# Performance work log

Measured on AMD Instinct MI355X. Metric: run time of the kernel, lower is better.

## Reference

```python
import jax, jax.numpy as jnp
import numpy as np

N = 50000   # nodes
E = 800000  # edges
D = 512     # channels (hidden_dim*2 == input_dim)
B = 64      # graphs in batch
L = 4       # GCN layers
OUT = 2
EPS = 1e-5


def setup_inputs() -> dict:
    key = jax.random.key(0)
    ks = jax.random.split(key, 12)
    x = jax.random.normal(ks[0], (N, D), jnp.float32)
    edge_index = jax.random.randint(ks[1], (2, E), 0, N, dtype=jnp.int64)
    batch = jnp.sort(jax.random.randint(ks[2], (N,), 0, B, dtype=jnp.int64))
    same_date = jax.random.randint(ks[3], (E,), 0, 2, dtype=jnp.int64)
    # parameters: 4 stacked GCNConv layers (same shape), BN stats, final linear
    Wc = jax.random.normal(ks[4], (L, D, D), jnp.float32) / np.float32(np.sqrt(D))
    bc = jax.random.normal(ks[5], (L, D), jnp.float32) * 0.01
    gamma = 1.0 + 0.1 * jax.random.normal(ks[6], (L, D), jnp.float32)
    beta = 0.1 * jax.random.normal(ks[7], (L, D), jnp.float32)
    rmean = 0.1 * jax.random.normal(ks[8], (L, D), jnp.float32)
    rvar = 0.5 + jax.random.uniform(ks[9], (L, D), jnp.float32)
    Wlin = jax.random.normal(ks[10], (2 * D, OUT), jnp.float32) / np.float32(np.sqrt(2 * D))
    blin = jnp.zeros((OUT,), jnp.float32)
    return {"x": x, "edge_index": edge_index, "batch": batch, "same_date": same_date,
            "Wc": Wc, "bc": bc, "gamma": gamma, "beta": beta, "rmean": rmean,
            "rvar": rvar, "Wlin": Wlin, "blin": blin}


def reference(x, edge_index, batch, same_date, Wc, bc, gamma, beta, rmean, rvar, Wlin, blin):
    # edge weights: 1.0 if same_date else 0.7
    w = jnp.where(same_date == 1, jnp.float32(1.0), jnp.float32(0.7))
    # GCN normalization with added self-loops (fill value 1.0)
    loops = jnp.arange(N, dtype=edge_index.dtype)
    row = jnp.concatenate([edge_index[0], loops])  # sources
    col = jnp.concatenate([edge_index[1], loops])  # targets
    ew = jnp.concatenate([w, jnp.ones((N,), jnp.float32)])
    deg = jax.ops.segment_sum(ew, col, num_segments=N)          # in-degree (weighted)
    dis = jax.lax.rsqrt(jnp.maximum(deg, EPS))                   # deg >= 1 from self-loops
    norm = dis[row] * ew * dis[col]                              # [E+N]

    h = x
    for i in range(L):
        hw = h @ Wc[i]                                           # [N, D]
        msg = hw[row] * norm[:, None]                            # gather + scale
        agg = jax.ops.segment_sum(msg, col, num_segments=N) + bc[i]
        # BatchNorm (inference: running stats) + ReLU; dropout is identity in eval
        h = gamma[i] * (agg - rmean[i]) * jax.lax.rsqrt(rvar[i] + EPS) + beta[i]
        h = jax.nn.relu(h)

    counts = jax.ops.segment_sum(jnp.ones((N,), jnp.float32), batch, num_segments=B)
    x_mean = jax.ops.segment_sum(h, batch, num_segments=B) / jnp.maximum(counts, 1.0)[:, None]
    x_max = jax.ops.segment_max(h, batch, num_segments=B)
    x_max = jnp.where(jnp.isfinite(x_max), x_max, 0.0)           # guard empty graphs
    z = jnp.concatenate([x_mean, x_max], axis=1) @ Wlin + blin   # [B, OUT]
    return jax.nn.log_softmax(z, axis=1)
```

## Files before the change

kernel.cpp:

```cpp
#include <hip/hip_runtime.h>
#include <hip/hip_bf16.h>

#define NN 50000
#define EE 800000
#define DD 512
#define BB 64
#define LL 4
#define OUTC 2
#define EPSV 1e-5f

#define MTG 64
#define BKG 64
#define HV8 (NN * DD / 8)

typedef _Float16 halfx8 __attribute__((ext_vector_type(8)));
typedef float floatx4 __attribute__((ext_vector_type(4)));
typedef float floatx2 __attribute__((ext_vector_type(2)));

#if defined(__has_builtin)
#if __has_builtin(__builtin_amdgcn_cvt_pk_f32_fp8) && __has_builtin(__builtin_amdgcn_cvt_pk_fp8_f32)
#define HW_FP8 1
#endif
#endif

#ifdef HW_FP8
__device__ __forceinline__ floatx2 f8x2_lo(unsigned int u) {
    return __builtin_amdgcn_cvt_pk_f32_fp8(u, 0);
}
__device__ __forceinline__ floatx2 f8x2_hi(unsigned int u) {
    return __builtin_amdgcn_cvt_pk_f32_fp8(u, 1);
}
__device__ __forceinline__ unsigned int f8_pack_lo(float a, float b, unsigned int old) {
    return (unsigned int)__builtin_amdgcn_cvt_pk_fp8_f32(a, b, (int)old, 0);
}
__device__ __forceinline__ unsigned int f8_pack_hi(float a, float b, unsigned int old) {
    return (unsigned int)__builtin_amdgcn_cvt_pk_fp8_f32(a, b, (int)old, 1);
}
__device__ __forceinline__ unsigned char f8_enc1(float v) {
    return (unsigned char)(__builtin_amdgcn_cvt_pk_fp8_f32(v, v, 0, 0) & 0xff);
}
#else
__device__ __forceinline__ float f8_dec1(unsigned int b) {
    unsigned int s = b & 0x80u, e = (b >> 3) & 15u, m = b & 7u;
    float v = e ? __uint_as_float(((e + 120u) << 23) | (m << 20))
                : (float)m * 0.001953125f;
    return s ? -v : v;
}
__device__ __forceinline__ floatx2 f8x2_lo(unsigned int u) {
    floatx2 r; r[0] = f8_dec1(u & 0xffu); r[1] = f8_dec1((u >> 8) & 0xffu); return r;
}
__device__ __forceinline__ floatx2 f8x2_hi(unsigned int u) {
    floatx2 r; r[0] = f8_dec1((u >> 16) & 0xffu); r[1] = f8_dec1((u >> 24) & 0xffu); return r;
}
__device__ __forceinline__ unsigned char f8_enc1(float x) {
    unsigned int s = (__float_as_uint(x) >> 24) & 0x80u;
    float a = fabsf(x);
    if (a < 0.015625f) {
        int m = (int)(a * 512.0f + 0.5f);
        return (unsigned char)(s | (unsigned int)m);
    }
    unsigned int ab = __float_as_uint(a);
    int e = (int)(ab >> 23) - 127;
    unsigned int m23 = ab & 0x7fffffu;
    unsigned int r = m23 + 0x7ffffu + ((m23 >> 20) & 1u);
    if (r >= 0x800000u) { e++; r -= 0x800000u; }
    unsigned int m = r >> 20;
    if (e > 8 || (e == 8 && m >= 7u)) return (unsigned char)(s | 0x7eu);
    return (unsigned char)(s | ((unsigned int)(e + 7) << 3) | m);
}
__device__ __forceinline__ unsigned int f8_pack_lo(float a, float b, unsigned int old) {
    return (old & 0xffff0000u) | (unsigned int)f8_enc1(a) | ((unsigned int)f8_enc1(b) << 8);
}
__device__ __forceinline__ unsigned int f8_pack_hi(float a, float b, unsigned int old) {
    return (old & 0x0000ffffu) | ((unsigned int)f8_enc1(a) << 16) | ((unsigned int)f8_enc1(b) << 24);
}
#endif

__device__ __forceinline__ floatx4 mfma16h(halfx8 a, halfx8 b, floatx4 c) {
    return __builtin_amdgcn_mfma_f32_16x16x32_f16(a, b, c, 0, 0, 0);
}

__device__ __forceinline__ void ldg2lds16(const _Float16* g, _Float16* l) {
    __builtin_amdgcn_global_load_lds(
        (const __attribute__((address_space(1))) unsigned int*)g,
        (__attribute__((address_space(3))) unsigned int*)l, 16, 0, 0);
}


__global__ void k_prep(const float* __restrict__ x, const float* __restrict__ Wc,
                       const int* __restrict__ ei, const int* __restrict__ sd,
                       const float* __restrict__ bc, const float* __restrict__ gamma,
                       const float* __restrict__ beta, const float* __restrict__ rmean,
                       const float* __restrict__ rvar,
                       unsigned char* __restrict__ X8, _Float16* __restrict__ WT,
                       unsigned long long* __restrict__ degcnt,
                       float* __restrict__ scb, float* __restrict__ shb) {
    int i = blockIdx.x * blockDim.x + threadIdx.x;
    if (i < HV8) {
        const float4* xp = (const float4*)x + (size_t)i * 2;
        float4 v0 = xp[0], v1 = xp[1];
        unsigned int u0 = 0, u1 = 0;
        u0 = f8_pack_lo(v0.x, v0.y, u0);
        u0 = f8_pack_hi(v0.z, v0.w, u0);
        u1 = f8_pack_lo(v1.x, v1.y, u1);
        u1 = f8_pack_hi(v1.z, v1.w, u1);
        uint2 q; q.x = u0; q.y = u1;
        ((uint2*)X8)[i] = q;
    }
    if (i < LL * DD * DD) {
        int l = i >> 18;
        int rem = i & ((DD * DD) - 1);
        int n = rem >> 9;
        int k = rem & (DD - 1);
        WT[(l << 18) + (n << 9) + (k ^ ((n & 7) << 3))] =
            (_Float16)Wc[(l << 18) + (k << 9) + n];
    }
    if (i < LL * DD) {
        float rs = rsqrtf(rvar[i] + EPSV);
        float scv = gamma[i] * rs;
        scb[i] = scv;
        shb[i] = scv * (bc[i] - rmean[i]) + beta[i];
    }
    if ((i & 3) == 0) {
        int e = i >> 2;
        if (e < EE) {
            int c = ei[EE + e];
            unsigned long long v =
                0x100000000ull + (unsigned long long)((sd[e] == 1) ? 10u : 7u);
            atomicAdd(&degcnt[c], v);
        }
    }
}

__global__ void k_scan1(const unsigned long long* __restrict__ degcnt,
                        int* __restrict__ rowptr, int* __restrict__ bsum,
                        float* __restrict__ dis, const int* __restrict__ batch,
                        int* __restrict__ gstart, int* __restrict__ gend) {
    __shared__ int sh[256];
    const int t = threadIdx.x;
    const int i = blockIdx.x * 256 + t;
    int cntv = 0;
    if (i < NN) {
        unsigned long long dc = degcnt[i];
        cntv = (int)(dc >> 32);
        float degv = 0.1f * (float)(unsigned int)(dc & 0xffffffffu);
        dis[i] = rsqrtf(fmaxf(degv + 1.0f, EPSV));
        int g = batch[i];
        int gp = (i == 0) ? -1 : batch[i - 1];
        if (g != gp) gstart[g] = i;
        int gn = (i == NN - 1) ? BB : batch[i + 1];
        if (g != gn) gend[g] = i + 1;
    }
    sh[t] = cntv;
    __syncthreads();
    for (int off = 1; off < 256; off <<= 1) {
        int y = (t >= off) ? sh[t - off] : 0;
        __syncthreads();
        if (t >= off) sh[t] += y;
        __syncthreads();
    }
    if (i < NN) rowptr[i] = sh[t] - cntv;
    if (t == 255) bsum[blockIdx.x] = sh[255];
}

__global__ void k_scan2(int* __restrict__ bsum, int* __restrict__ rowptr, int nb) {
    __shared__ int sh[256];
    const int t = threadIdx.x;
    int v = (t < nb) ? bsum[t] : 0;
    sh[t] = v;
    __syncthreads();
    for (int off = 1; off < 256; off <<= 1) {
        int y = (t >= off) ? sh[t - off] : 0;
        __syncthreads();
        if (t >= off) sh[t] += y;
        __syncthreads();
    }
    if (t < nb) bsum[t] = sh[t] - v;
    if (t == 255) rowptr[NN] = sh[255];
}

__global__ void k_scan3(int* __restrict__ rowptr, const int* __restrict__ bsum) {
    int i = blockIdx.x * blockDim.x + threadIdx.x;
    if (i < NN) rowptr[i] += bsum[i >> 8];
}

__global__ void k_fill(const int* __restrict__ ei, const int* __restrict__ sd,
                       const float* __restrict__ dis, const int* __restrict__ rowptr,
                       int* __restrict__ fill, int* __restrict__ srcs,
                       float* __restrict__ enorm) {
    int e = blockIdx.x * blockDim.x + threadIdx.x;
    if (e >= EE) return;
    int s = ei[e];
    int c = ei[EE + e];
    float w = (sd[e] == 1) ? 1.0f : 0.7f;
    int p = rowptr[c] + atomicAdd(&fill[c], 1);
    srcs[p] = s;
    enorm[p] = dis[s] * w * dis[c];
}

__launch_bounds__(256)
__global__ void k_agg(const unsigned char* __restrict__ h8, const int* __restrict__ rowptr,
                      const int* __restrict__ srcs, const float* __restrict__ enorm,
                      const float* __restrict__ dis, _Float16* __restrict__ S) {
    const int n = blockIdx.x * 4 + (threadIdx.x >> 6);
    const int lane = threadIdx.x & 63;
    if (n >= NN) return;
    const float dn = dis[n];
    const float sw = dn * dn;
    uint2 q = ((const uint2*)(h8 + (size_t)n * DD))[lane];
    floatx2 acc[4];
    acc[0] = f8x2_lo(q.x) * sw;
    acc[1] = f8x2_hi(q.x) * sw;
    acc[2] = f8x2_lo(q.y) * sw;
    acc[3] = f8x2_hi(q.y) * sw;
    const int s0 = rowptr[n], s1 = rowptr[n + 1];
    int i = s0;
    for (; i + 8 <= s1; i += 8) {
        int sv[8];
        float wv[8];
        uint2 qv[8];
#pragma unroll
        for (int u = 0; u < 8; u++) { sv[u] = srcs[i + u]; wv[u] = enorm[i + u]; }
#pragma unroll
        for (int u = 0; u < 8; u++)
            qv[u] = ((const uint2*)(h8 + (size_t)sv[u] * DD))[lane];
#pragma unroll
        for (int u = 0; u < 8; u++) {
            acc[0] += f8x2_lo(qv[u].x) * wv[u];
            acc[1] += f8x2_hi(qv[u].x) * wv[u];
            acc[2] += f8x2_lo(qv[u].y) * wv[u];
            acc[3] += f8x2_hi(qv[u].y) * wv[u];
        }
    }
    for (; i + 4 <= s1; i += 4) {
        int sv[4];
        float wv[4];
        uint2 qv[4];
#pragma unroll
        for (int u = 0; u < 4; u++) { sv[u] = srcs[i + u]; wv[u] = enorm[i + u]; }
#pragma unroll
        for (int u = 0; u < 4; u++)
            qv[u] = ((const uint2*)(h8 + (size_t)sv[u] * DD))[lane];
#pragma unroll
        for (int u = 0; u < 4; u++) {
            acc[0] += f8x2_lo(qv[u].x) * wv[u];
            acc[1] += f8x2_hi(qv[u].x) * wv[u];
            acc[2] += f8x2_lo(qv[u].y) * wv[u];
            acc[3] += f8x2_hi(qv[u].y) * wv[u];
        }
    }
    for (; i < s1; i++) {
        uint2 qb = ((const uint2*)(h8 + (size_t)srcs[i] * DD))[lane];
        const float wn = enorm[i];
        acc[0] += f8x2_lo(qb.x) * wn;
        acc[1] += f8x2_hi(qb.x) * wn;
        acc[2] += f8x2_lo(qb.y) * wn;
        acc[3] += f8x2_hi(qb.y) * wn;
    }
    halfx8 hv;
#pragma unroll
    for (int k = 0; k < 4; k++) {
        hv[2 * k] = (_Float16)acc[k][0];
        hv[2 * k + 1] = (_Float16)acc[k][1];
    }
    ((halfx8*)(S + (size_t)n * DD))[lane ^ (n & 7)] = hv;
}

template <int OUT8>
__launch_bounds__(512)
__global__ void k_gemm(const _Float16* __restrict__ A,
                       const _Float16* __restrict__ B,
                       const float* __restrict__ sc, const float* __restrict__ sh,
                       _Float16* __restrict__ C16, unsigned char* __restrict__ C8) {
    __shared__ _Float16 sA[MTG * BKG];
    __shared__ _Float16 sB[512 * BKG];

    const int t = threadIdx.x;
    const int wid = t >> 6;
    const int lane = t & 63;
    const int l15 = lane & 15;
    const int quad = lane >> 4;
    const int m0 = blockIdx.x * MTG;
    const int wc = wid * 64;
    const int key = l15 & 7;

    int arow = m0 + (t >> 3);
    if (arow > NN - 1) arow = NN - 1;
    const _Float16* gA = A + (size_t)arow * DD + (t & 7) * 8;
    _Float16* lA = sA + t * 8;
    const _Float16* gB = B + (size_t)(t >> 3) * DD + (t & 7) * 8;
    _Float16* lB = sB + t * 8;

    floatx4 acc[4][4];
#pragma unroll
    for (int i = 0; i < 4; i++)
#pragma unroll
        for (int j = 0; j < 4; j++) acc[i][j] = (floatx4){0.f, 0.f, 0.f, 0.f};

    for (int k0 = 0; k0 < DD; k0 += BKG) {
        __syncthreads();
        ldg2lds16(gA + k0, lA);
#pragma unroll
        for (int r = 0; r < 8; r++)
            ldg2lds16(gB + (size_t)r * 64 * DD + k0, lB + r * 4096);
        __syncthreads();

#pragma unroll
        for (int cc = 0; cc < 2; cc++) {
            halfx8 a[4], b[4];
            const int goff = ((cc * 4 + quad) ^ key) * 8;
#pragma unroll
            for (int i = 0; i < 4; i++)
                a[i] = *(const halfx8*)&sA[(i * 16 + l15) * BKG + goff];
#pragma unroll
            for (int j = 0; j < 4; j++)
                b[j] = *(const halfx8*)&sB[(wc + j * 16 + l15) * BKG + goff];
#pragma unroll
            for (int i = 0; i < 4; i++)
#pragma unroll
                for (int j = 0; j < 4; j++)
                    acc[i][j] = mfma16h(a[i], b[j], acc[i][j]);
        }
    }

#pragma unroll
    for (int j = 0; j < 4; j++) {
        const int gcol = wc + j * 16 + l15;
        const float scv = sc[gcol];
        const float shv = sh[gcol];
#pragma unroll
        for (int i = 0; i < 4; i++) {
            const int rbase = m0 + i * 16 + quad * 4;
#pragma unroll
            for (int r = 0; r < 4; r++) {
                const int grow = rbase + r;
                if (grow < NN) {
                    float v = fmaxf(fmaf(scv, acc[i][j][r], shv), 0.f);
                    if (OUT8)
                        C8[(size_t)grow * DD + gcol] = f8_enc1(v);
                    else
                        C16[(size_t)grow * DD + gcol] = (_Float16)v;
                }
            }
        }
    }
}

__launch_bounds__(512)
__global__ void k_pool(const _Float16* __restrict__ H,
                       const int* __restrict__ gstart, const int* __restrict__ gend,
                       float* __restrict__ psum, unsigned int* __restrict__ pmax) {
    const int g = blockIdx.x;
    const int sl = blockIdx.y;
    const int c = threadIdx.x;
    const int s0 = gstart[g], e0 = gend[g];
    if (e0 <= s0) return;
    const int len = e0 - s0;
    const int chunk = (len + 7) >> 3;
    const int lo = s0 + sl * chunk;
    const int hi = min(lo + chunk, e0);
    float sum = 0.f, mx = 0.f;
    for (int n = lo; n < hi; n++) {
        float v = (float)H[(size_t)n * DD + c];
        sum += v;
        mx = fmaxf(mx, v);
    }
    if (lo < hi) {
        atomicAdd(&psum[g * DD + c], sum);
        atomicMax(&pmax[g * DD + c], __float_as_uint(fmaxf(mx, 0.f)));
    }
}

__launch_bounds__(64)
__global__ void k_final(const float* __restrict__ psum, const unsigned int* __restrict__ pmax,
                        const int* __restrict__ gstart, const int* __restrict__ gend,
                        const float* __restrict__ Wlin, const float* __restrict__ blin,
                        float* __restrict__ out) {
    const int g = blockIdx.x;
    const int lane = threadIdx.x;
    int cntg = gend[g] - gstart[g];
    if (cntg < 1) cntg = 1;
    const float inv = 1.0f / (float)cntg;
    float z0 = 0.f, z1 = 0.f;
#pragma unroll
    for (int j = 0; j < 8; j++) {
        const int k = j * 64 + lane;
        float mean = psum[g * DD + k] * inv;
        float mx = __uint_as_float(pmax[g * DD + k]);
        z0 += mean * Wlin[k * OUTC + 0] + mx * Wlin[(DD + k) * OUTC + 0];
        z1 += mean * Wlin[k * OUTC + 1] + mx * Wlin[(DD + k) * OUTC + 1];
    }
#pragma unroll
    for (int off = 32; off > 0; off >>= 1) {
        z0 += __shfl_down(z0, off);
        z1 += __shfl_down(z1, off);
    }
    if (lane == 0) {
        z0 += blin[0];
        z1 += blin[1];
        float m = fmaxf(z0, z1);
        float ls = m + logf(expf(z0 - m) + expf(z1 - m));
        out[g * OUTC + 0] = z0 - ls;
        out[g * OUTC + 1] = z1 - ls;
    }
}

extern "C" void kernel_launch(void* const* d_in, const int* in_sizes, int n_in,
                              void* d_out, int out_size, void* d_ws, size_t ws_size,
                              hipStream_t stream) {
    const float* x = (const float*)d_in[0];
    const int* ei = (const int*)d_in[1];
    const int* batch = (const int*)d_in[2];
    const int* sd = (const int*)d_in[3];
    const float* Wc = (const float*)d_in[4];
    const float* bc = (const float*)d_in[5];
    const float* gamma = (const float*)d_in[6];
    const float* beta = (const float*)d_in[7];
    const float* rmean = (const float*)d_in[8];
    const float* rvar = (const float*)d_in[9];
    const float* Wlin = (const float*)d_in[10];
    const float* blin = (const float*)d_in[11];
    float* out = (float*)d_out;

    char* p = (char*)d_ws;
    auto alloc = [&](size_t bytes) {
        char* r = p;
        p += (bytes + 255) & ~(size_t)255;
        return r;
    };
    _Float16* S = (_Float16*)alloc((size_t)NN * DD * 2);
    unsigned char* X8a = (unsigned char*)alloc((size_t)NN * DD);
    unsigned char* X8b = (unsigned char*)alloc((size_t)NN * DD);
    _Float16* WT = (_Float16*)alloc((size_t)LL * DD * DD * 2);
    float* scb = (float*)alloc(LL * DD * 4);
    float* shb = (float*)alloc(LL * DD * 4);
    char* zbase = p;
    unsigned long long* degcnt = (unsigned long long*)alloc(NN * 8);
    float* dis = (float*)alloc(NN * 4);
    int* fill = (int*)alloc(NN * 4);
    int* rowptr = (int*)alloc((NN + 1) * 4);
    int* bsum = (int*)alloc(256 * 4);
    int* srcs = (int*)alloc(EE * 4);
    float* enorm = (float*)alloc(EE * 4);
    int* gstart = (int*)alloc(BB * 4);
    int* gend = (int*)alloc(BB * 4);
    float* psum = (float*)alloc(BB * DD * 4);
    unsigned int* pmax = (unsigned int*)alloc(BB * DD * 4);
    size_t zbytes = (size_t)(p - zbase);
    (void)ws_size; (void)in_sizes; (void)n_in; (void)out_size;

    const int nb256 = (NN + 255) / 256;
    const int eb256 = (EE + 255) / 256;

    hipMemsetAsync(zbase, 0, zbytes, stream);
    k_prep<<<(HV8 + 255) / 256, 256, 0, stream>>>(x, Wc, ei, sd, bc, gamma, beta,
                                                  rmean, rvar, X8a, WT, degcnt, scb, shb);
    k_scan1<<<nb256, 256, 0, stream>>>(degcnt, rowptr, bsum, dis, batch, gstart, gend);
    k_scan2<<<1, 256, 0, stream>>>(bsum, rowptr, nb256);
    k_scan3<<<nb256, 256, 0, stream>>>(rowptr, bsum);
    k_fill<<<eb256, 256, 0, stream>>>(ei, sd, dis, rowptr, fill, srcs, enorm);

    const int ggrid = (NN + MTG - 1) / MTG;
    unsigned char* bufs[2] = {X8a, X8b};
    int cur = 0;
    for (int l = 0; l < LL; l++) {
        k_agg<<<(NN + 3) / 4, 256, 0, stream>>>(bufs[cur], rowptr, srcs, enorm, dis, S);
        if (l < LL - 1)
            k_gemm<1><<<ggrid, 512, 0, stream>>>(S, WT + (size_t)l * DD * DD,
                                                 scb + l * DD, shb + l * DD,
                                                 nullptr, bufs[cur ^ 1]);
        else
            k_gemm<0><<<ggrid, 512, 0, stream>>>(S, WT + (size_t)l * DD * DD,
                                                 scb + l * DD, shb + l * DD,
                                                 S, nullptr);
        cur ^= 1;
    }

    k_pool<<<dim3(BB, 8), 512, 0, stream>>>(S, gstart, gend, psum, pmax);
    k_final<<<BB, 64, 0, stream>>>(psum, pmax, gstart, gend, Wlin, blin, out);
}
```

Baseline: 724.3 us.

## Stage full A tile in LDS and stream B weights from global into registers

The GEMM now loads the whole 64x512 activation tile into shared memory once, with a single barrier, instead of re-staging A and B tiles every K step with two barriers each. Each wave reads its own weight columns straight from global memory (expected to stay L2-resident) into registers, using a one-stage software prefetch between half-steps. The weight transpose drops its LDS swizzle since B no longer goes through shared memory, and launch bounds gain an occupancy hint. The risk is that the B loads now wait on L2 latency, which the shallow prefetch may not hide, and every block re-reads the full weight matrix from cache.

After: 850.6 us. 17.4% more time.

```diff
diff --git a/kernel.cpp b/kernel.cpp
--- a/kernel.cpp
+++ b/kernel.cpp
@@ -10,7 +10,6 @@
 #define EPSV 1e-5f
 
 #define MTG 64
-#define BKG 64
 #define HV8 (NN * DD / 8)
 
 typedef _Float16 halfx8 __attribute__((ext_vector_type(8)));
@@ -112,8 +111,7 @@
         int rem = i & ((DD * DD) - 1);
         int n = rem >> 9;
         int k = rem & (DD - 1);
-        WT[(l << 18) + (n << 9) + (k ^ ((n & 7) << 3))] =
-            (_Float16)Wc[(l << 18) + (k << 9) + n];
+        WT[i] = (_Float16)Wc[(l << 18) + (k << 9) + n];
     }
     if (i < LL * DD) {
         float rs = rsqrtf(rvar[i] + EPSV);
@@ -267,13 +265,12 @@
 }
 
 template <int OUT8>
-__launch_bounds__(512)
+__launch_bounds__(512, 4)
 __global__ void k_gemm(const _Float16* __restrict__ A,
                        const _Float16* __restrict__ B,
                        const float* __restrict__ sc, const float* __restrict__ sh,
                        _Float16* __restrict__ C16, unsigned char* __restrict__ C8) {
-    __shared__ _Float16 sA[MTG * BKG];
-    __shared__ _Float16 sB[512 * BKG];
+    __shared__ _Float16 sA[MTG * DD];
 
     const int t = threadIdx.x;
     const int wid = t >> 6;
@@ -284,12 +281,14 @@
     const int wc = wid * 64;
     const int key = l15 & 7;
 
-    int arow = m0 + (t >> 3);
-    if (arow > NN - 1) arow = NN - 1;
-    const _Float16* gA = A + (size_t)arow * DD + (t & 7) * 8;
-    _Float16* lA = sA + t * 8;
-    const _Float16* gB = B + (size_t)(t >> 3) * DD + (t & 7) * 8;
-    _Float16* lB = sB + t * 8;
+#pragma unroll
+    for (int r = 0; r < 8; r++) {
+        int arow = m0 + r * 8 + wid;
+        if (arow > NN - 1) arow = NN - 1;
+        ldg2lds16(A + (size_t)arow * DD + (t & 63) * 8, sA + r * 4096 + t * 8);
+    }
+
+    const _Float16* gB0 = B + (size_t)(wc + l15) * DD + quad * 8;
 
     floatx4 acc[4][4];
 #pragma unroll
@@ -297,30 +296,42 @@
 #pragma unroll
         for (int j = 0; j < 4; j++) acc[i][j] = (floatx4){0.f, 0.f, 0.f, 0.f};
 
-    for (int k0 = 0; k0 < DD; k0 += BKG) {
-        __syncthreads();
-        ldg2lds16(gA + k0, lA);
-#pragma unroll
-        for (int r = 0; r < 8; r++)
-            ldg2lds16(gB + (size_t)r * 64 * DD + k0, lB + r * 4096);
-        __syncthreads();
-
-#pragma unroll
-        for (int cc = 0; cc < 2; cc++) {
-            halfx8 a[4], b[4];
-            const int goff = ((cc * 4 + quad) ^ key) * 8;
-#pragma unroll
-            for (int i = 0; i < 4; i++)
-                a[i] = *(const halfx8*)&sA[(i * 16 + l15) * BKG + goff];
+    halfx8 b0[4], b1[4];
+#pragma unroll
+    for (int j = 0; j < 4; j++)
+        b0[j] = *(const halfx8*)(gB0 + (size_t)(j * 16) * DD);
+
+    __syncthreads();
+
+#pragma unroll
+    for (int k0 = 0; k0 < DD; k0 += 64) {
+        halfx8 a[4];
+#pragma unroll
+        for (int j = 0; j < 4; j++)
+            b1[j] = *(const halfx8*)(gB0 + (size_t)(j * 16) * DD + k0 + 32);
+#pragma unroll
+        for (int i = 0; i < 4; i++)
+            a[i] = *(const halfx8*)
+                &sA[(i * 16 + l15) * DD + ((((k0 >> 3) + quad) ^ key) << 3)];
+#pragma unroll
+        for (int i = 0; i < 4; i++)
 #pragma unroll
             for (int j = 0; j < 4; j++)
-                b[j] = *(const halfx8*)&sB[(wc + j * 16 + l15) * BKG + goff];
-#pragma unroll
-            for (int i = 0; i < 4; i++)
-#pragma unroll
-                for (int j = 0; j < 4; j++)
-                    acc[i][j] = mfma16h(a[i], b[j], acc[i][j]);
+                acc[i][j] = mfma16h(a[i], b0[j], acc[i][j]);
+        if (k0 + 64 < DD) {
+#pragma unroll
+            for (int j = 0; j < 4; j++)
+                b0[j] = *(const halfx8*)(gB0 + (size_t)(j * 16) * DD + k0 + 64);
         }
+#pragma unroll
+        for (int i = 0; i < 4; i++)
+            a[i] = *(const halfx8*)
+                &sA[(i * 16 + l15) * DD + (((((k0 + 32) >> 3) + quad) ^ key) << 3)];
+#pragma unroll
+        for (int i = 0; i < 4; i++)
+#pragma unroll
+            for (int j = 0; j < 4; j++)
+                acc[i][j] = mfma16h(a[i], b1[j], acc[i][j]);
     }
 
 #pragma unroll
```
